# Performance work log

Measured on AMD Instinct MI355X. Metric: run time of the kernel, lower is better.

## Reference

```python
import jax, jax.numpy as jnp
import numpy as np

COORD = 5.0
NOOBJ = 0.5


def _reflat(x):
    # torch: flatten(x.transpose(0,1), start_dim=1).transpose(0,1) -> [B*S*S, C]
    C = x.shape[1]
    return jnp.moveaxis(x, 1, -1).reshape(-1, C)


def setup_inputs() -> dict:
    key = jax.random.key(0)
    k1, k2 = jax.random.split(key)
    B, C, S = 256, 25, 64
    inp = jax.random.uniform(k1, (B, C, S, S), dtype=jnp.float32)
    tgt = jax.random.uniform(k2, (B, C, S, S), dtype=jnp.float32)
    return {"input": inp, "target": tgt}


def _iou(b1, b2, blocks):
    # vectorized, detached IoU between predicted and target boxes, per row
    b1 = jax.lax.stop_gradient(b1)
    b2 = jax.lax.stop_gradient(b2)
    c1 = b1[:, :2] / blocks
    c2 = b2[:, :2] / blocks
    x1a, x2a = c1[:, 0] - b1[:, 2] / 2, c1[:, 0] + b1[:, 2] / 2
    y1a, y2a = c1[:, 1] - b1[:, 3] / 2, c1[:, 1] + b1[:, 3] / 2
    x1b, x2b = c2[:, 0] - b2[:, 2] / 2, c2[:, 0] + b2[:, 2] / 2
    y1b, y2b = c2[:, 1] - b2[:, 3] / 2, c2[:, 1] + b2[:, 3] / 2
    dx = jnp.minimum(x2a, x2b) - jnp.maximum(x1a, x1b)
    dy = jnp.minimum(y2a, y2b) - jnp.maximum(y1a, y1b)
    inter = dx * dy
    union = b1[:, 2] * b1[:, 3] + b2[:, 2] * b2[:, 3] - inter
    pos = (dx > 0) & (dy > 0)
    return jnp.where(pos, inter / jnp.where(pos, union, 1.0), 0.0)


def reference(input, target):
    blocks = target.shape[-1]
    t = _reflat(target)  # [N, C]
    p = _reflat(input)   # [N, C]
    m = (t[:, 4] > 0).astype(p.dtype)  # responsible-cell mask [N]
    iou = _iou(p[:, :4], t[:, :4], blocks)  # detached target confidence
    sp = jnp.sqrt(p[:, 2:4])
    st = jnp.sqrt(t[:, 2:4])
    m2 = m[:, None]
    loss = COORD * jnp.sum(m2 * jnp.square(p[:, :2] - t[:, :2]))
    loss += COORD * jnp.sum(m2 * jnp.square(sp - st))
    loss += jnp.sum(m * jnp.square(p[:, 4] - iou))
    loss += NOOBJ * jnp.sum((1.0 - m) * jnp.square(p[:, 4]))
    loss += jnp.sum(m2 * jnp.square(p[:, 5:] - t[:, 5:]))
    return loss
```

## Files before the change

### kernel.cpp

```cpp
#include <hip/hip_runtime.h>


#define COORD 5.0f
#define NOOBJ 0.5f

constexpr int B = 256;
constexpr int C = 25;
constexpr int S = 64;
constexpr int SS = S * S;
constexpr int CH_STRIDE4 = SS / 4;
constexpr int IMG_STRIDE4 = C * CH_STRIDE4;
constexpr int N4 = B * SS / 4;

constexpr int THREADS = 256;
constexpr int CLASS_CH = 20;
constexpr int CLASS_ITEMS = CLASS_CH * N4;
constexpr int CLASS_BLOCKS = 2560;
constexpr int CLASS_THREADS = CLASS_BLOCKS * THREADS;
constexpr int CLASS_IPT = CLASS_ITEMS / CLASS_THREADS;
constexpr int BOX_BLOCKS = N4 / THREADS;
constexpr int TOTAL_BLOCKS = CLASS_BLOCKS + BOX_BLOCKS;

__device__ __forceinline__ float comp(const float4 v, int k) {
    switch (k) {
        case 0: return v.x;
        case 1: return v.y;
        case 2: return v.z;
        default: return v.w;
    }
}

__global__ void zero_out_kernel(float* out) { out[0] = 0.0f; }

__global__ __launch_bounds__(256) void yolo_loss_kernel(
        const float4* __restrict__ in, const float4* __restrict__ tg,
        float* __restrict__ out) {
    float acc = 0.0f;

    if (blockIdx.x < CLASS_BLOCKS) {
        const int t = blockIdx.x * THREADS + threadIdx.x;
        #pragma unroll
        for (int i = 0; i < CLASS_IPT; i += 2) {
            const int it0 = t + (i + 0) * CLASS_THREADS;
            const int it1 = t + (i + 1) * CLASS_THREADS;
            const int c0 = 5 + (it0 >> 18);
            const int c1 = 5 + (it1 >> 18);
            const int g0 = it0 & (N4 - 1);
            const int g1 = it1 & (N4 - 1);
            const int base0 = (g0 >> 10) * IMG_STRIDE4 + (g0 & 1023);
            const int base1 = (g1 >> 10) * IMG_STRIDE4 + (g1 & 1023);
            const float4 pv0 = in[base0 + c0 * CH_STRIDE4];
            const float4 tv0 = tg[base0 + c0 * CH_STRIDE4];
            const float4 mk0 = tg[base0 + 4 * CH_STRIDE4];
            const float4 pv1 = in[base1 + c1 * CH_STRIDE4];
            const float4 tv1 = tg[base1 + c1 * CH_STRIDE4];
            const float4 mk1 = tg[base1 + 4 * CH_STRIDE4];
            float d;
            d = pv0.x - tv0.x; acc += (mk0.x > 0.0f) ? d * d : 0.0f;
            d = pv0.y - tv0.y; acc += (mk0.y > 0.0f) ? d * d : 0.0f;
            d = pv0.z - tv0.z; acc += (mk0.z > 0.0f) ? d * d : 0.0f;
            d = pv0.w - tv0.w; acc += (mk0.w > 0.0f) ? d * d : 0.0f;
            d = pv1.x - tv1.x; acc += (mk1.x > 0.0f) ? d * d : 0.0f;
            d = pv1.y - tv1.y; acc += (mk1.y > 0.0f) ? d * d : 0.0f;
            d = pv1.z - tv1.z; acc += (mk1.z > 0.0f) ? d * d : 0.0f;
            d = pv1.w - tv1.w; acc += (mk1.w > 0.0f) ? d * d : 0.0f;
        }
    } else {
        const int g = (blockIdx.x - CLASS_BLOCKS) * THREADS + threadIdx.x;
        const int base = (g >> 10) * IMG_STRIDE4 + (g & 1023);

        const float4 p0 = in[base + 0 * CH_STRIDE4];
        const float4 p1 = in[base + 1 * CH_STRIDE4];
        const float4 p2 = in[base + 2 * CH_STRIDE4];
        const float4 p3 = in[base + 3 * CH_STRIDE4];
        const float4 p4 = in[base + 4 * CH_STRIDE4];
        const float4 t0 = tg[base + 0 * CH_STRIDE4];
        const float4 t1 = tg[base + 1 * CH_STRIDE4];
        const float4 t2 = tg[base + 2 * CH_STRIDE4];
        const float4 t3 = tg[base + 3 * CH_STRIDE4];
        const float4 t4 = tg[base + 4 * CH_STRIDE4];

        const float invBlocks = 1.0f / (float)S;
        #pragma unroll
        for (int k = 0; k < 4; ++k) {
            const float px = comp(p0, k), py = comp(p1, k);
            const float pw = comp(p2, k), ph = comp(p3, k);
            const float pc = comp(p4, k);
            const float tx = comp(t0, k), ty = comp(t1, k);
            const float tw = comp(t2, k), th = comp(t3, k);
            const float tc = comp(t4, k);
            const float m = (tc > 0.0f) ? 1.0f : 0.0f;

            const float c1x = px * invBlocks, c1y = py * invBlocks;
            const float c2x = tx * invBlocks, c2y = ty * invBlocks;
            const float x1a = c1x - pw * 0.5f, x2a = c1x + pw * 0.5f;
            const float y1a = c1y - ph * 0.5f, y2a = c1y + ph * 0.5f;
            const float x1b = c2x - tw * 0.5f, x2b = c2x + tw * 0.5f;
            const float y1b = c2y - th * 0.5f, y2b = c2y + th * 0.5f;
            const float dx = fminf(x2a, x2b) - fmaxf(x1a, x1b);
            const float dy = fminf(y2a, y2b) - fmaxf(y1a, y1b);
            const float inter = dx * dy;
            const float uni = pw * ph + tw * th - inter;
            const bool pos = (dx > 0.0f) && (dy > 0.0f);
            const float iou = pos ? (inter / uni) : 0.0f;

            const float ex = px - tx, ey = py - ty;
            acc += COORD * m * (ex * ex + ey * ey);
            const float sw = sqrtf(pw) - sqrtf(tw);
            const float sh = sqrtf(ph) - sqrtf(th);
            acc += COORD * m * (sw * sw + sh * sh);
            const float ec = pc - iou;
            acc += m * ec * ec;
            acc += NOOBJ * (1.0f - m) * (pc * pc);
        }
    }

    #pragma unroll
    for (int off = 32; off > 0; off >>= 1)
        acc += __shfl_down(acc, off, 64);

    __shared__ float smem[4];
    const int lane = threadIdx.x & 63;
    const int wid = threadIdx.x >> 6;
    if (lane == 0) smem[wid] = acc;
    __syncthreads();
    if (threadIdx.x == 0) {
        const float s = smem[0] + smem[1] + smem[2] + smem[3];
        atomicAdd(out, s);
    }
}

extern "C" void kernel_launch(void* const* d_in, const int* in_sizes, int n_in,
                              void* d_out, int out_size, void* d_ws, size_t ws_size,
                              hipStream_t stream) {
    const float4* in = (const float4*)d_in[0];
    const float4* tg = (const float4*)d_in[1];
    float* out = (float*)d_out;

    zero_out_kernel<<<1, 1, 0, stream>>>(out);

    yolo_loss_kernel<<<TOTAL_BLOCKS, THREADS, 0, stream>>>(in, tg, out);
}
```

Baseline: 227.6 us.

## Precompute byte mask in workspace to shrink class-loop mask reads

Adds a pre-pass kernel that turns the target confidence channel into a compact byte mask stored in workspace. The class-channel loop then reads 4 bytes per cell instead of a float4, which cuts the repeated mask traffic across the 20 class channels. The loop is also restructured to issue 4 loads per batch, and launch bounds now request 4 blocks per CU. In exchange there is an extra kernel launch and an extra pass over channel 4. The path depends on whether the workspace is large enough, and falls back to the old float mask reads otherwise.

```diff
diff --git a/kernel.cpp b/kernel.cpp
--- a/kernel.cpp
+++ b/kernel.cpp
@@ -16,10 +16,11 @@
 constexpr int CLASS_CH = 20;
 constexpr int CLASS_ITEMS = CLASS_CH * N4;
 constexpr int CLASS_BLOCKS = 2560;
-constexpr int CLASS_THREADS = CLASS_BLOCKS * THREADS;
-constexpr int CLASS_IPT = CLASS_ITEMS / CLASS_THREADS;
+constexpr int CLASS_THREADS_TOT = CLASS_BLOCKS * THREADS;
+constexpr int CLASS_IPT = CLASS_ITEMS / CLASS_THREADS_TOT;
 constexpr int BOX_BLOCKS = N4 / THREADS;
 constexpr int TOTAL_BLOCKS = CLASS_BLOCKS + BOX_BLOCKS;
+constexpr int MASK_BYTES = N4 * 4;
 
 __device__ __forceinline__ float comp(const float4 v, int k) {
     switch (k) {
@@ -32,38 +33,49 @@
 
 __global__ void zero_out_kernel(float* out) { out[0] = 0.0f; }
 
-__global__ __launch_bounds__(256) void yolo_loss_kernel(
+__global__ __launch_bounds__(256) void mask_kernel(
+        const float4* __restrict__ tg, uchar4* __restrict__ mask) {
+    const int g = blockIdx.x * 256 + threadIdx.x;
+    const float4 t4 = tg[(g >> 10) * IMG_STRIDE4 + (g & 1023) + 4 * CH_STRIDE4];
+    mask[g] = make_uchar4(t4.x > 0.0f, t4.y > 0.0f, t4.z > 0.0f, t4.w > 0.0f);
+}
+
+__global__ __launch_bounds__(256, 4) void yolo_loss_kernel(
         const float4* __restrict__ in, const float4* __restrict__ tg,
+        const uchar4* __restrict__ mask,
         float* __restrict__ out) {
     float acc = 0.0f;
 
     if (blockIdx.x < CLASS_BLOCKS) {
         const int t = blockIdx.x * THREADS + threadIdx.x;
         #pragma unroll
-        for (int i = 0; i < CLASS_IPT; i += 2) {
-            const int it0 = t + (i + 0) * CLASS_THREADS;
-            const int it1 = t + (i + 1) * CLASS_THREADS;
-            const int c0 = 5 + (it0 >> 18);
-            const int c1 = 5 + (it1 >> 18);
-            const int g0 = it0 & (N4 - 1);
-            const int g1 = it1 & (N4 - 1);
-            const int base0 = (g0 >> 10) * IMG_STRIDE4 + (g0 & 1023);
-            const int base1 = (g1 >> 10) * IMG_STRIDE4 + (g1 & 1023);
-            const float4 pv0 = in[base0 + c0 * CH_STRIDE4];
-            const float4 tv0 = tg[base0 + c0 * CH_STRIDE4];
-            const float4 mk0 = tg[base0 + 4 * CH_STRIDE4];
-            const float4 pv1 = in[base1 + c1 * CH_STRIDE4];
-            const float4 tv1 = tg[base1 + c1 * CH_STRIDE4];
-            const float4 mk1 = tg[base1 + 4 * CH_STRIDE4];
-            float d;
-            d = pv0.x - tv0.x; acc += (mk0.x > 0.0f) ? d * d : 0.0f;
-            d = pv0.y - tv0.y; acc += (mk0.y > 0.0f) ? d * d : 0.0f;
-            d = pv0.z - tv0.z; acc += (mk0.z > 0.0f) ? d * d : 0.0f;
-            d = pv0.w - tv0.w; acc += (mk0.w > 0.0f) ? d * d : 0.0f;
-            d = pv1.x - tv1.x; acc += (mk1.x > 0.0f) ? d * d : 0.0f;
-            d = pv1.y - tv1.y; acc += (mk1.y > 0.0f) ? d * d : 0.0f;
-            d = pv1.z - tv1.z; acc += (mk1.z > 0.0f) ? d * d : 0.0f;
-            d = pv1.w - tv1.w; acc += (mk1.w > 0.0f) ? d * d : 0.0f;
+        for (int i = 0; i < CLASS_IPT; i += 4) {
+            float4 pv[4], tv[4];
+            uchar4 mk[4];
+            #pragma unroll
+            for (int u = 0; u < 4; ++u) {
+                const int itm = t + (i + u) * CLASS_THREADS_TOT;
+                const int c = 5 + (itm >> 18);
+                const int g = itm & (N4 - 1);
+                const int base = (g >> 10) * IMG_STRIDE4 + (g & 1023);
+                pv[u] = in[base + c * CH_STRIDE4];
+                tv[u] = tg[base + c * CH_STRIDE4];
+                if (mask) {
+                    mk[u] = mask[g];
+                } else {
+                    const float4 t4 = tg[base + 4 * CH_STRIDE4];
+                    mk[u] = make_uchar4(t4.x > 0.0f, t4.y > 0.0f,
+                                        t4.z > 0.0f, t4.w > 0.0f);
+                }
+            }
+            #pragma unroll
+            for (int u = 0; u < 4; ++u) {
+                float d;
+                d = pv[u].x - tv[u].x; if (mk[u].x) acc += d * d;
+                d = pv[u].y - tv[u].y; if (mk[u].y) acc += d * d;
+                d = pv[u].z - tv[u].z; if (mk[u].z) acc += d * d;
+                d = pv[u].w - tv[u].w; if (mk[u].w) acc += d * d;
+            }
         }
     } else {
         const int g = (blockIdx.x - CLASS_BLOCKS) * THREADS + threadIdx.x;
@@ -139,5 +151,11 @@
 
     zero_out_kernel<<<1, 1, 0, stream>>>(out);
 
-    yolo_loss_kernel<<<TOTAL_BLOCKS, THREADS, 0, stream>>>(in, tg, out);
+    uchar4* mask = nullptr;
+    if (d_ws != nullptr && ws_size >= (size_t)MASK_BYTES) {
+        mask = (uchar4*)d_ws;
+        mask_kernel<<<N4 / 256, 256, 0, stream>>>(tg, mask);
+    }
+
+    yolo_loss_kernel<<<TOTAL_BLOCKS, THREADS, 0, stream>>>(in, tg, mask, out);
 }
```

Result: no change. 230.1 us (+1.1%).

## Group class channels per thread to share mask load and cut redundant reads

Applied to the files above, without the earlier changes.

Class-channel work is remapped so each thread handles one pixel-quad across five consecutive class channels. It loads the mask channel once per five channels instead of once per channel, which removes most of the redundant mask traffic. The launch uses more blocks (4096 class blocks) with fewer items each, plus a launch-bounds occupancy hint and fma-based masked accumulation. This increases the number of blocks and atomics and changes the load pattern from cross-thread strided to per-thread multi-channel.

```diff
diff --git a/kernel.cpp b/kernel.cpp
--- a/kernel.cpp
+++ b/kernel.cpp
@@ -13,11 +13,8 @@
 constexpr int N4 = B * SS / 4;
 
 constexpr int THREADS = 256;
-constexpr int CLASS_CH = 20;
-constexpr int CLASS_ITEMS = CLASS_CH * N4;
-constexpr int CLASS_BLOCKS = 2560;
-constexpr int CLASS_THREADS = CLASS_BLOCKS * THREADS;
-constexpr int CLASS_IPT = CLASS_ITEMS / CLASS_THREADS;
+constexpr int CSETS = 4;
+constexpr int CLASS_BLOCKS = CSETS * N4 / THREADS;
 constexpr int BOX_BLOCKS = N4 / THREADS;
 constexpr int TOTAL_BLOCKS = CLASS_BLOCKS + BOX_BLOCKS;
 
@@ -30,41 +27,72 @@
     }
 }
 
+__device__ __forceinline__ void block_reduce_atomic(float acc, float* out) {
+    #pragma unroll
+    for (int off = 32; off > 0; off >>= 1)
+        acc += __shfl_down(acc, off, 64);
+    __shared__ float smem[4];
+    const int lane = threadIdx.x & 63;
+    const int wid = threadIdx.x >> 6;
+    if (lane == 0) smem[wid] = acc;
+    __syncthreads();
+    if (threadIdx.x == 0) {
+        atomicAdd(out, smem[0] + smem[1] + smem[2] + smem[3]);
+    }
+}
+
 __global__ void zero_out_kernel(float* out) { out[0] = 0.0f; }
 
-__global__ __launch_bounds__(256) void yolo_loss_kernel(
+__global__ __launch_bounds__(256, 4) void yolo_loss_kernel(
         const float4* __restrict__ in, const float4* __restrict__ tg,
         float* __restrict__ out) {
     float acc = 0.0f;
 
     if (blockIdx.x < CLASS_BLOCKS) {
         const int t = blockIdx.x * THREADS + threadIdx.x;
-        #pragma unroll
-        for (int i = 0; i < CLASS_IPT; i += 2) {
-            const int it0 = t + (i + 0) * CLASS_THREADS;
-            const int it1 = t + (i + 1) * CLASS_THREADS;
-            const int c0 = 5 + (it0 >> 18);
-            const int c1 = 5 + (it1 >> 18);
-            const int g0 = it0 & (N4 - 1);
-            const int g1 = it1 & (N4 - 1);
-            const int base0 = (g0 >> 10) * IMG_STRIDE4 + (g0 & 1023);
-            const int base1 = (g1 >> 10) * IMG_STRIDE4 + (g1 & 1023);
-            const float4 pv0 = in[base0 + c0 * CH_STRIDE4];
-            const float4 tv0 = tg[base0 + c0 * CH_STRIDE4];
-            const float4 mk0 = tg[base0 + 4 * CH_STRIDE4];
-            const float4 pv1 = in[base1 + c1 * CH_STRIDE4];
-            const float4 tv1 = tg[base1 + c1 * CH_STRIDE4];
-            const float4 mk1 = tg[base1 + 4 * CH_STRIDE4];
-            float d;
-            d = pv0.x - tv0.x; acc += (mk0.x > 0.0f) ? d * d : 0.0f;
-            d = pv0.y - tv0.y; acc += (mk0.y > 0.0f) ? d * d : 0.0f;
-            d = pv0.z - tv0.z; acc += (mk0.z > 0.0f) ? d * d : 0.0f;
-            d = pv0.w - tv0.w; acc += (mk0.w > 0.0f) ? d * d : 0.0f;
-            d = pv1.x - tv1.x; acc += (mk1.x > 0.0f) ? d * d : 0.0f;
-            d = pv1.y - tv1.y; acc += (mk1.y > 0.0f) ? d * d : 0.0f;
-            d = pv1.z - tv1.z; acc += (mk1.z > 0.0f) ? d * d : 0.0f;
-            d = pv1.w - tv1.w; acc += (mk1.w > 0.0f) ? d * d : 0.0f;
-        }
+        const int cset = t >> 18;
+        const int g = t & (N4 - 1);
+        const int base = (g >> 10) * IMG_STRIDE4 + (g & 1023);
+        const int cbase = base + (5 + cset * 5) * CH_STRIDE4;
+
+        const float4 t4  = tg[base + 4 * CH_STRIDE4];
+        const float4 pv0 = in[cbase + 0 * CH_STRIDE4];
+        const float4 tv0 = tg[cbase + 0 * CH_STRIDE4];
+        const float4 pv1 = in[cbase + 1 * CH_STRIDE4];
+        const float4 tv1 = tg[cbase + 1 * CH_STRIDE4];
+        const float4 pv2 = in[cbase + 2 * CH_STRIDE4];
+        const float4 tv2 = tg[cbase + 2 * CH_STRIDE4];
+        const float4 pv3 = in[cbase + 3 * CH_STRIDE4];
+        const float4 tv3 = tg[cbase + 3 * CH_STRIDE4];
+        const float4 pv4 = in[cbase + 4 * CH_STRIDE4];
+        const float4 tv4 = tg[cbase + 4 * CH_STRIDE4];
+
+        const float mx = t4.x > 0.0f ? 1.0f : 0.0f;
+        const float my = t4.y > 0.0f ? 1.0f : 0.0f;
+        const float mz = t4.z > 0.0f ? 1.0f : 0.0f;
+        const float mw = t4.w > 0.0f ? 1.0f : 0.0f;
+
+        float d;
+        d = pv0.x - tv0.x; acc = fmaf(mx * d, d, acc);
+        d = pv0.y - tv0.y; acc = fmaf(my * d, d, acc);
+        d = pv0.z - tv0.z; acc = fmaf(mz * d, d, acc);
+        d = pv0.w - tv0.w; acc = fmaf(mw * d, d, acc);
+        d = pv1.x - tv1.x; acc = fmaf(mx * d, d, acc);
+        d = pv1.y - tv1.y; acc = fmaf(my * d, d, acc);
+        d = pv1.z - tv1.z; acc = fmaf(mz * d, d, acc);
+        d = pv1.w - tv1.w; acc = fmaf(mw * d, d, acc);
+        d = pv2.x - tv2.x; acc = fmaf(mx * d, d, acc);
+        d = pv2.y - tv2.y; acc = fmaf(my * d, d, acc);
+        d = pv2.z - tv2.z; acc = fmaf(mz * d, d, acc);
+        d = pv2.w - tv2.w; acc = fmaf(mw * d, d, acc);
+        d = pv3.x - tv3.x; acc = fmaf(mx * d, d, acc);
+        d = pv3.y - tv3.y; acc = fmaf(my * d, d, acc);
+        d = pv3.z - tv3.z; acc = fmaf(mz * d, d, acc);
+        d = pv3.w - tv3.w; acc = fmaf(mw * d, d, acc);
+        d = pv4.x - tv4.x; acc = fmaf(mx * d, d, acc);
+        d = pv4.y - tv4.y; acc = fmaf(my * d, d, acc);
+        d = pv4.z - tv4.z; acc = fmaf(mz * d, d, acc);
+        d = pv4.w - tv4.w; acc = fmaf(mw * d, d, acc);
     } else {
         const int g = (blockIdx.x - CLASS_BLOCKS) * THREADS + threadIdx.x;
         const int base = (g >> 10) * IMG_STRIDE4 + (g & 1023);
@@ -115,19 +143,7 @@
         }
     }
 
-    #pragma unroll
-    for (int off = 32; off > 0; off >>= 1)
-        acc += __shfl_down(acc, off, 64);
-
-    __shared__ float smem[4];
-    const int lane = threadIdx.x & 63;
-    const int wid = threadIdx.x >> 6;
-    if (lane == 0) smem[wid] = acc;
-    __syncthreads();
-    if (threadIdx.x == 0) {
-        const float s = smem[0] + smem[1] + smem[2] + smem[3];
-        atomicAdd(out, s);
-    }
+    block_reduce_atomic(acc, out);
 }
 
 extern "C" void kernel_launch(void* const* d_in, const int* in_sizes, int n_in,
```

Measured after the change: 228.2 us. No clear change (+0.3%).
